# Kernel tuning notes

Hardware: AMD Instinct MI355X
Metric: run time of the kernel (lower is better)

## Reference

```python
import jax, jax.numpy as jnp
import numpy as np

B, L, D = 32, 4096, 1024


def setup_inputs() -> dict:
    key = jax.random.key(0)
    k_h, k_idx, k_w1, k_w2 = jax.random.split(key, 4)
    h = jax.random.normal(k_h, (B, L, D), dtype=jnp.float32)
    # 4 sorted positions per sample: [s1, e1, s2, e2]; +arange*2 guarantees
    # strict increase and a non-empty context region (s2 > e1 + 1).
    raw = jnp.sort(jax.random.randint(k_idx, (B, 4), 0, L - 10), axis=-1)
    pts = raw + jnp.arange(4, dtype=raw.dtype) * 2
    span1_idx = pts[:, 0:2].reshape(B, 1, 2).astype(jnp.int64)
    span2_idx = pts[:, 2:4].reshape(B, 1, 2).astype(jnp.int64)
    scale1 = 1.0 / np.sqrt(3 * D)
    scale2 = 1.0 / np.sqrt(D)
    W1 = jax.random.normal(k_w1, (3 * D, D), dtype=jnp.float32) * scale1
    b1 = jnp.zeros((D,), dtype=jnp.float32)
    W2 = jax.random.normal(k_w2, (D, D), dtype=jnp.float32) * scale2
    b2 = jnp.zeros((D,), dtype=jnp.float32)
    return {"h": h, "span1_idx": span1_idx, "span2_idx": span2_idx,
            "W1": W1, "b1": b1, "W2": W2, "b2": b2}


def _masked_mean(h, lo, hi_excl):
    # mean of h[b, lo[b]:hi_excl[b], :] over the length axis, vectorized
    pos = jnp.arange(h.shape[1])  # [L]
    mask = ((pos[None, :] >= lo[:, None]) & (pos[None, :] < hi_excl[:, None])).astype(h.dtype)  # [B,L]
    cnt = jnp.maximum(mask.sum(axis=1, keepdims=True), 1.0)  # [B,1]
    return jnp.einsum('bl,bld->bd', mask, h) / cnt  # [B,D]


def reference(h, span1_idx, span2_idx, W1, b1, W2, b2):
    s1, e1 = span1_idx[:, 0, 0], span1_idx[:, 0, 1]
    s2, e2 = span2_idx[:, 0, 0], span2_idx[:, 0, 1]
    span1_rep = _masked_mean(h, s1, e1 + 1)          # span tokens inclusive
    span2_rep = _masked_mean(h, s2, e2 + 1)
    context_rep = _masked_mean(h, e1 + 1, s2)        # tokens strictly between spans
    combined = jnp.concatenate([span1_rep, context_rep, span2_rep], axis=-1)  # [B,3D]
    hmid = jax.nn.relu(combined @ W1 + b1)
    out = hmid @ W2 + b2
    return out[:, None, :]  # [B,1,D]
```

## Files before the change

kernel.cpp:

```cpp
#include <hip/hip_runtime.h>

#define BB 32
#define LL 4096
#define DD 1024
#define G1 1024
#define K2_TILE 64
#define K3_TILE 32

static __device__ __forceinline__ int imax(int a, int b) { return a > b ? a : b; }
static __device__ __forceinline__ int imin(int a, int b) { return a < b ? a : b; }

__global__ __launch_bounds__(256) void k0_zero(float* __restrict__ sums_hmid,
                                               float* __restrict__ out) {
    const int i = blockIdx.x * 256 + threadIdx.x;
    const float4 z = make_float4(0.f, 0.f, 0.f, 0.f);
    if (i < 32768) ((float4*)sums_hmid)[i] = z;
    else ((float4*)out)[i - 32768] = z;
}

static __device__ __forceinline__ void accum_rows_add(const float* __restrict__ hb,
                                                      int beg, int end, float4& acc) {
    float4 a0 = make_float4(0.f, 0.f, 0.f, 0.f);
    float4 a1 = a0, a2 = a0, a3 = a0, a4 = a0, a5 = a0, a6 = a0, a7 = a0;
    int l = beg;
    for (; l + 8 <= end; l += 8) {
        float4 v0 = *(const float4*)(hb + (size_t)(l + 0) * DD);
        float4 v1 = *(const float4*)(hb + (size_t)(l + 1) * DD);
        float4 v2 = *(const float4*)(hb + (size_t)(l + 2) * DD);
        float4 v3 = *(const float4*)(hb + (size_t)(l + 3) * DD);
        float4 v4 = *(const float4*)(hb + (size_t)(l + 4) * DD);
        float4 v5 = *(const float4*)(hb + (size_t)(l + 5) * DD);
        float4 v6 = *(const float4*)(hb + (size_t)(l + 6) * DD);
        float4 v7 = *(const float4*)(hb + (size_t)(l + 7) * DD);
        a0.x += v0.x; a0.y += v0.y; a0.z += v0.z; a0.w += v0.w;
        a1.x += v1.x; a1.y += v1.y; a1.z += v1.z; a1.w += v1.w;
        a2.x += v2.x; a2.y += v2.y; a2.z += v2.z; a2.w += v2.w;
        a3.x += v3.x; a3.y += v3.y; a3.z += v3.z; a3.w += v3.w;
        a4.x += v4.x; a4.y += v4.y; a4.z += v4.z; a4.w += v4.w;
        a5.x += v5.x; a5.y += v5.y; a5.z += v5.z; a5.w += v5.w;
        a6.x += v6.x; a6.y += v6.y; a6.z += v6.z; a6.w += v6.w;
        a7.x += v7.x; a7.y += v7.y; a7.z += v7.z; a7.w += v7.w;
    }
    for (; l + 4 <= end; l += 4) {
        float4 v0 = *(const float4*)(hb + (size_t)(l + 0) * DD);
        float4 v1 = *(const float4*)(hb + (size_t)(l + 1) * DD);
        float4 v2 = *(const float4*)(hb + (size_t)(l + 2) * DD);
        float4 v3 = *(const float4*)(hb + (size_t)(l + 3) * DD);
        a0.x += v0.x; a0.y += v0.y; a0.z += v0.z; a0.w += v0.w;
        a1.x += v1.x; a1.y += v1.y; a1.z += v1.z; a1.w += v1.w;
        a2.x += v2.x; a2.y += v2.y; a2.z += v2.z; a2.w += v2.w;
        a3.x += v3.x; a3.y += v3.y; a3.z += v3.z; a3.w += v3.w;
    }
    for (; l < end; ++l) {
        float4 v = *(const float4*)(hb + (size_t)l * DD);
        a0.x += v.x; a0.y += v.y; a0.z += v.z; a0.w += v.w;
    }
    acc.x += ((a0.x + a1.x) + (a2.x + a3.x)) + ((a4.x + a5.x) + (a6.x + a7.x));
    acc.y += ((a0.y + a1.y) + (a2.y + a3.y)) + ((a4.y + a5.y) + (a6.y + a7.y));
    acc.z += ((a0.z + a1.z) + (a2.z + a3.z)) + ((a4.z + a5.z) + (a6.z + a7.z));
    acc.w += ((a0.w + a1.w) + (a2.w + a3.w)) + ((a4.w + a5.w) + (a6.w + a7.w));
}

__global__ __launch_bounds__(256) void k1_sums(const float* __restrict__ h,
                                               const int* __restrict__ sp1,
                                               const int* __restrict__ sp2,
                                               float* __restrict__ sums) {
    const int tid = threadIdx.x;

    int NC = 0;
#pragma unroll
    for (int b = 0; b < BB; ++b)
        NC += sp2[2 * b + 1] - sp1[2 * b] + 1;

    const int q = NC / G1, r = NC % G1;
    const int bk = blockIdx.x;
    int c0 = bk * q + imin(bk, r);
    const int c1 = c0 + q + (bk < r ? 1 : 0);
    if (c0 >= c1) return;

    int b = 0, base = 0, s1, e1, s2, e2, len;
    for (;; ++b) {
        s1 = sp1[2 * b]; e1 = sp1[2 * b + 1];
        s2 = sp2[2 * b]; e2 = sp2[2 * b + 1];
        len = e2 - s1 + 1;
        if (c0 < base + len) break;
        base += len;
    }

    for (;;) {
        const int cend = imin(c1, base + len);
        const int rb = s1 + (c0 - base);
        const int re = s1 + (cend - base);
        const float* hb = h + (size_t)b * LL * DD + (size_t)tid * 4;
        float* dstb = sums + (size_t)b * 3 * DD + (size_t)tid * 4;
        const int lo[3] = {rb, imax(rb, e1 + 1), imax(rb, s2)};
        const int hi[3] = {imin(re, e1 + 1), imin(re, s2), re};
#pragma unroll
        for (int s = 0; s < 3; ++s) {
            if (lo[s] < hi[s]) {
                float4 acc = make_float4(0.f, 0.f, 0.f, 0.f);
                accum_rows_add(hb, lo[s], hi[s], acc);
                float* d = dstb + s * DD;
                atomicAdd(d + 0, acc.x); atomicAdd(d + 1, acc.y);
                atomicAdd(d + 2, acc.z); atomicAdd(d + 3, acc.w);
            }
        }
        c0 = cend;
        if (c0 >= c1) break;
        base += len; ++b;
        s1 = sp1[2 * b]; e1 = sp1[2 * b + 1];
        s2 = sp2[2 * b]; e2 = sp2[2 * b + 1];
        len = e2 - s1 + 1;
    }
}

__global__ __launch_bounds__(256) void k2_gemm1(const float* __restrict__ sums,
                                                const int* __restrict__ sp1,
                                                const int* __restrict__ sp2,
                                                const float* __restrict__ W1,
                                                float* __restrict__ hmid) {
    __shared__ float cl[K2_TILE * BB];
    __shared__ float icl[BB];
    const int tid = threadIdx.x;
    const int j = blockIdx.x * 256 + tid;
    const int k0 = blockIdx.y * K2_TILE;
    const int seg = k0 / DD;

    if (tid < BB) {
        const int b = tid;
        const int s1 = sp1[2 * b], e1 = sp1[2 * b + 1];
        const int s2 = sp2[2 * b], e2 = sp2[2 * b + 1];
        const int cnt = (seg == 0) ? (e1 + 1 - s1) : (seg == 1) ? (s2 - e1 - 1) : (e2 + 1 - s2);
        icl[b] = 1.0f / (float)imax(cnt, 1);
    }
    __syncthreads();
    for (int i = tid; i < K2_TILE * BB; i += 256) {
        const int kk = i / BB;
        const int b = i % BB;
        cl[i] = sums[(size_t)b * (3 * DD) + (k0 + kk)] * icl[b];
    }
    __syncthreads();

    float acc[BB];
#pragma unroll
    for (int b = 0; b < BB; ++b) acc[b] = 0.f;

    const float* w = W1 + (size_t)k0 * DD + j;
#pragma unroll 4
    for (int kk = 0; kk < K2_TILE; ++kk) {
        const float wv = w[(size_t)kk * DD];
        const float4* c4 = (const float4*)(cl + kk * BB);
#pragma unroll
        for (int qq = 0; qq < BB / 4; ++qq) {
            float4 c = c4[qq];
            acc[4 * qq + 0] = fmaf(c.x, wv, acc[4 * qq + 0]);
            acc[4 * qq + 1] = fmaf(c.y, wv, acc[4 * qq + 1]);
            acc[4 * qq + 2] = fmaf(c.z, wv, acc[4 * qq + 2]);
            acc[4 * qq + 3] = fmaf(c.w, wv, acc[4 * qq + 3]);
        }
    }
#pragma unroll
    for (int b = 0; b < BB; ++b) atomicAdd(&hmid[(size_t)b * DD + j], acc[b]);
}

__global__ __launch_bounds__(256) void k3_gemm2(const float* __restrict__ hmid,
                                                const float* __restrict__ b1,
                                                const float* __restrict__ W2,
                                                const float* __restrict__ b2,
                                                float* __restrict__ out) {
    __shared__ float al[K3_TILE * BB];
    const int tid = threadIdx.x;
    const int j = blockIdx.x * 256 + tid;
    const int k0 = blockIdx.y * K3_TILE;

    for (int i = tid; i < K3_TILE * BB; i += 256) {
        const int kk = i / BB;
        const int b = i % BB;
        const float v = hmid[(size_t)b * DD + (k0 + kk)] + b1[k0 + kk];
        al[i] = fmaxf(v, 0.f);
    }
    __syncthreads();

    float acc[BB];
    const float bias = (blockIdx.y == 0) ? b2[j] : 0.f;
#pragma unroll
    for (int b = 0; b < BB; ++b) acc[b] = bias;

    const float* w = W2 + (size_t)k0 * DD + j;
#pragma unroll 4
    for (int kk = 0; kk < K3_TILE; ++kk) {
        const float wv = w[(size_t)kk * DD];
        const float4* c4 = (const float4*)(al + kk * BB);
#pragma unroll
        for (int qq = 0; qq < BB / 4; ++qq) {
            float4 c = c4[qq];
            acc[4 * qq + 0] = fmaf(c.x, wv, acc[4 * qq + 0]);
            acc[4 * qq + 1] = fmaf(c.y, wv, acc[4 * qq + 1]);
            acc[4 * qq + 2] = fmaf(c.z, wv, acc[4 * qq + 2]);
            acc[4 * qq + 3] = fmaf(c.w, wv, acc[4 * qq + 3]);
        }
    }
#pragma unroll
    for (int b = 0; b < BB; ++b) atomicAdd(&out[(size_t)b * DD + j], acc[b]);
}

extern "C" void kernel_launch(void* const* d_in, const int* in_sizes, int n_in,
                              void* d_out, int out_size, void* d_ws, size_t ws_size,
                              hipStream_t stream) {
    const float* h = (const float*)d_in[0];
    const int* sp1 = (const int*)d_in[1];
    const int* sp2 = (const int*)d_in[2];
    const float* W1 = (const float*)d_in[3];
    const float* b1 = (const float*)d_in[4];
    const float* W2 = (const float*)d_in[5];
    const float* b2 = (const float*)d_in[6];
    float* out = (float*)d_out;

    float* sums = (float*)d_ws;
    float* hmid = sums + BB * 3 * DD;

    k0_zero<<<160, 256, 0, stream>>>((float*)d_ws, out);
    k1_sums<<<G1, 256, 0, stream>>>(h, sp1, sp2, sums);
    k2_gemm1<<<dim3(DD / 256, 3 * DD / K2_TILE), 256, 0, stream>>>(sums, sp1, sp2, W1, hmid);
    k3_gemm2<<<dim3(DD / 256, DD / K3_TILE), 256, 0, stream>>>(hmid, b1, W2, b2, out);
}
```

Before: 111.9 us.

## Retile GEMM kernels so each thread computes 8 batch rows over 64 columns

Both small GEMM kernels are reorganized. Each block now covers 64 output columns and splits the 32 batch rows across 4 thread groups of 8, instead of one thread holding all 32 batch accumulators for 256 columns. The K tiles grow to 96 and 64, and the scale factors for all three segments are precomputed so a tile can span segment boundaries. This lowers register pressure and cuts atomics per block. The cost is that each W element is now loaded by four threads, and shared memory is read as scalars rather than float4.

```diff
diff --git a/kernel.cpp b/kernel.cpp
--- a/kernel.cpp
+++ b/kernel.cpp
@@ -4,8 +4,8 @@
 #define LL 4096
 #define DD 1024
 #define G1 1024
-#define K2_TILE 64
-#define K3_TILE 32
+#define K2T 96
+#define K3T 64
 
 static __device__ __forceinline__ int imax(int a, int b) { return a > b ? a : b; }
 static __device__ __forceinline__ int imin(int a, int b) { return a < b ? a : b; }
@@ -119,48 +119,51 @@
                                                 const int* __restrict__ sp2,
                                                 const float* __restrict__ W1,
                                                 float* __restrict__ hmid) {
-    __shared__ float cl[K2_TILE * BB];
-    __shared__ float icl[BB];
+    __shared__ float cl[BB * K2T];
+    __shared__ float icl[3 * BB];
     const int tid = threadIdx.x;
-    const int j = blockIdx.x * 256 + tid;
-    const int k0 = blockIdx.y * K2_TILE;
-    const int seg = k0 / DD;
-
-    if (tid < BB) {
-        const int b = tid;
+    const int k0 = blockIdx.y * K2T;
+
+    if (tid < 3 * BB) {
+        const int s = tid >> 5, b = tid & 31;
         const int s1 = sp1[2 * b], e1 = sp1[2 * b + 1];
         const int s2 = sp2[2 * b], e2 = sp2[2 * b + 1];
-        const int cnt = (seg == 0) ? (e1 + 1 - s1) : (seg == 1) ? (s2 - e1 - 1) : (e2 + 1 - s2);
-        icl[b] = 1.0f / (float)imax(cnt, 1);
+        const int cnt = (s == 0) ? (e1 + 1 - s1) : (s == 1) ? (s2 - e1 - 1) : (e2 + 1 - s2);
+        icl[tid] = 1.0f / (float)imax(cnt, 1);
     }
     __syncthreads();
-    for (int i = tid; i < K2_TILE * BB; i += 256) {
-        const int kk = i / BB;
-        const int b = i % BB;
-        cl[i] = sums[(size_t)b * (3 * DD) + (k0 + kk)] * icl[b];
+    for (int i = tid; i < BB * K2T; i += 256) {
+        const int b = i / K2T, kk = i - b * K2T;
+        const int k = k0 + kk;
+        cl[i] = sums[(size_t)b * (3 * DD) + k] * icl[(k >> 10) * BB + b];
     }
     __syncthreads();
 
-    float acc[BB];
-#pragma unroll
-    for (int b = 0; b < BB; ++b) acc[b] = 0.f;
-
+    const int tx = tid & 63, ty = tid >> 6;
+    const int j = blockIdx.x * 64 + tx;
+    const float* c = cl + (ty * 8) * K2T;
     const float* w = W1 + (size_t)k0 * DD + j;
-#pragma unroll 4
-    for (int kk = 0; kk < K2_TILE; ++kk) {
-        const float wv = w[(size_t)kk * DD];
-        const float4* c4 = (const float4*)(cl + kk * BB);
-#pragma unroll
-        for (int qq = 0; qq < BB / 4; ++qq) {
-            float4 c = c4[qq];
-            acc[4 * qq + 0] = fmaf(c.x, wv, acc[4 * qq + 0]);
-            acc[4 * qq + 1] = fmaf(c.y, wv, acc[4 * qq + 1]);
-            acc[4 * qq + 2] = fmaf(c.z, wv, acc[4 * qq + 2]);
-            acc[4 * qq + 3] = fmaf(c.w, wv, acc[4 * qq + 3]);
+
+    float acc[8];
+#pragma unroll
+    for (int u = 0; u < 8; ++u) acc[u] = 0.f;
+
+    for (int kk = 0; kk < K2T; kk += 4) {
+        const float w0 = w[(size_t)(kk + 0) * DD];
+        const float w1 = w[(size_t)(kk + 1) * DD];
+        const float w2 = w[(size_t)(kk + 2) * DD];
+        const float w3 = w[(size_t)(kk + 3) * DD];
+#pragma unroll
+        for (int u = 0; u < 8; ++u) {
+            acc[u] = fmaf(c[u * K2T + kk + 0], w0, acc[u]);
+            acc[u] = fmaf(c[u * K2T + kk + 1], w1, acc[u]);
+            acc[u] = fmaf(c[u * K2T + kk + 2], w2, acc[u]);
+            acc[u] = fmaf(c[u * K2T + kk + 3], w3, acc[u]);
         }
     }
 #pragma unroll
-    for (int b = 0; b < BB; ++b) atomicAdd(&hmid[(size_t)b * DD + j], acc[b]);
+    for (int u = 0; u < 8; ++u)
+        atomicAdd(&hmid[(size_t)(ty * 8 + u) * DD + j], acc[u]);
 }
 
 __global__ __launch_bounds__(256) void k3_gemm2(const float* __restrict__ hmid,
@@ -168,40 +171,42 @@
                                                 const float* __restrict__ W2,
                                                 const float* __restrict__ b2,
                                                 float* __restrict__ out) {
-    __shared__ float al[K3_TILE * BB];
+    __shared__ float al[BB * K3T];
     const int tid = threadIdx.x;
-    const int j = blockIdx.x * 256 + tid;
-    const int k0 = blockIdx.y * K3_TILE;
-
-    for (int i = tid; i < K3_TILE * BB; i += 256) {
-        const int kk = i / BB;
-        const int b = i % BB;
-        const float v = hmid[(size_t)b * DD + (k0 + kk)] + b1[k0 + kk];
-        al[i] = fmaxf(v, 0.f);
+    const int k0 = blockIdx.y * K3T;
+
+    for (int i = tid; i < BB * K3T; i += 256) {
+        const int b = i >> 6, kk = i & 63;
+        al[i] = fmaxf(hmid[(size_t)b * DD + (k0 + kk)] + b1[k0 + kk], 0.f);
     }
     __syncthreads();
 
-    float acc[BB];
+    const int tx = tid & 63, ty = tid >> 6;
+    const int j = blockIdx.x * 64 + tx;
+    const float* a = al + (ty * 8) * K3T;
+    const float* w = W2 + (size_t)k0 * DD + j;
+
+    float acc[8];
     const float bias = (blockIdx.y == 0) ? b2[j] : 0.f;
 #pragma unroll
-    for (int b = 0; b < BB; ++b) acc[b] = bias;
-
-    const float* w = W2 + (size_t)k0 * DD + j;
-#pragma unroll 4
-    for (int kk = 0; kk < K3_TILE; ++kk) {
-        const float wv = w[(size_t)kk * DD];
-        const float4* c4 = (const float4*)(al + kk * BB);
-#pragma unroll
-        for (int qq = 0; qq < BB / 4; ++qq) {
-            float4 c = c4[qq];
-            acc[4 * qq + 0] = fmaf(c.x, wv, acc[4 * qq + 0]);
-            acc[4 * qq + 1] = fmaf(c.y, wv, acc[4 * qq + 1]);
-            acc[4 * qq + 2] = fmaf(c.z, wv, acc[4 * qq + 2]);
-            acc[4 * qq + 3] = fmaf(c.w, wv, acc[4 * qq + 3]);
+    for (int u = 0; u < 8; ++u) acc[u] = bias;
+
+    for (int kk = 0; kk < K3T; kk += 4) {
+        const float w0 = w[(size_t)(kk + 0) * DD];
+        const float w1 = w[(size_t)(kk + 1) * DD];
+        const float w2 = w[(size_t)(kk + 2) * DD];
+        const float w3 = w[(size_t)(kk + 3) * DD];
+#pragma unroll
+        for (int u = 0; u < 8; ++u) {
+            acc[u] = fmaf(a[u * K3T + kk + 0], w0, acc[u]);
+            acc[u] = fmaf(a[u * K3T + kk + 1], w1, acc[u]);
+            acc[u] = fmaf(a[u * K3T + kk + 2], w2, acc[u]);
+            acc[u] = fmaf(a[u * K3T + kk + 3], w3, acc[u]);
         }
     }
 #pragma unroll
-    for (int b = 0; b < BB; ++b) atomicAdd(&out[(size_t)b * DD + j], acc[b]);
+    for (int u = 0; u < 8; ++u)
+        atomicAdd(&out[(size_t)(ty * 8 + u) * DD + j], acc[u]);
 }
 
 extern "C" void kernel_launch(void* const* d_in, const int* in_sizes, int n_in,
@@ -221,6 +226,6 @@
 
     k0_zero<<<160, 256, 0, stream>>>((float*)d_ws, out);
     k1_sums<<<G1, 256, 0, stream>>>(h, sp1, sp2, sums);
-    k2_gemm1<<<dim3(DD / 256, 3 * DD / K2_TILE), 256, 0, stream>>>(sums, sp1, sp2, W1, hmid);
-    k3_gemm2<<<dim3(DD / 256, DD / K3_TILE), 256, 0, stream>>>(hmid, b1, W2, b2, out);
-}
+    k2_gemm1<<<dim3(DD / 64, 3 * DD / K2T), 256, 0, stream>>>(sums, sp1, sp2, W1, hmid);
+    k3_gemm2<<<dim3(DD / 64, DD / K3T), 256, 0, stream>>>(hmid, b1, W2, b2, out);
+}
```

After: 101.8 us. -9.0%, faster.
